# Kernel optimization log

Measured on AMD Instinct MI355X. Metric: run time of the kernel, lower is better.

The kernel has to match this reference:

```python
import jax, jax.numpy as jnp
import numpy as np

NB, FD, NR, L = 4, 128, 4, 4
CUT, CUT3, NE = 5.0, 4.0, 108
N_ATOMS, N_EDGES, N_ANGLES, N_GRAPHS = 8000, 200000, 400000, 100
BONDS_PER, ANGLES_PER = 2000, 4000

def swish(x):
    return x * jax.nn.sigmoid(x)

def cutoff_fn(r, rc):
    x = r / rc
    return 1.0 - 6.0 * x**5 + 15.0 * x**4 - 10.0 * x**3

def rbf(r):
    # smooth Bessel basis, [E, NR+1]
    n = jnp.arange(1, NR + 2, dtype=r.dtype)
    return jnp.sqrt(2.0 / CUT) * jnp.sin(n * jnp.pi * r[:, None] / CUT) / r[:, None]

def shrb(r, cos_t):
    # spherical-harmonic (Legendre, l=0..3) x radial Bessel (n=1..4) -> [A, 16]
    n = jnp.arange(1, NR + 1, dtype=r.dtype)
    rad = jnp.sin(n * jnp.pi * r[:, None] / CUT3) / r[:, None]
    ang = jnp.stack([jnp.ones_like(cos_t), cos_t, 0.5 * (3.0 * cos_t**2 - 1.0), 0.5 * (5.0 * cos_t**3 - 3.0 * cos_t)], axis=1)
    feat = (rad[:, :, None] * ang[:, None, :]).reshape(r.shape[0], NR * L)
    return feat * cutoff_fn(r, CUT3)[:, None]

def setup_inputs() -> dict:
    key = jax.random.key(0)
    ks = jax.random.split(key, 24)
    def nrm(k, shape, fan):
        return jax.random.normal(k, shape, jnp.float32) / np.sqrt(fan).astype(np.float32)
    return {
        'atomic_numbers': jax.random.randint(ks[0], (N_ATOMS,), 0, NE, jnp.int32),
        'edge_index': jax.random.randint(ks[1], (2, N_EDGES), 0, N_ATOMS, jnp.int32),
        'edge_dist': jax.random.uniform(ks[2], (N_EDGES,), jnp.float32, 0.5, CUT),
        'three_body_indices': jax.random.randint(ks[3], (N_ANGLES, 2), 0, BONDS_PER, jnp.int32),
        'norm_ik': jax.random.uniform(ks[4], (N_ANGLES,), jnp.float32, 0.5, CUT3),
        'cos_angles': jax.random.uniform(ks[5], (N_ANGLES,), jnp.float32, -1.0, 1.0),
        'total_num_bonds': jnp.full((N_GRAPHS,), BONDS_PER, jnp.int32),
        'total_num_angles': jnp.full((N_GRAPHS,), ANGLES_PER, jnp.int32),
        'emb': nrm(ks[6], (NE, FD), 1.0),
        'W_enc': nrm(ks[7], (NR + 1, FD), NR + 1), 'b_enc': jnp.zeros((FD,), jnp.float32),
        'W_angle': nrm(ks[8], (NB, NR * L, FD), NR * L),
        'Wg': nrm(ks[9], (NB, FD, FD), FD), 'bg': jnp.zeros((NB, FD), jnp.float32),
        'W_tb': nrm(ks[10], (NB, FD, FD), FD), 'b_tb': jnp.zeros((NB, FD), jnp.float32),
        'We1': nrm(ks[11], (NB, 3 * FD, FD), 3 * FD), 'be1': jnp.zeros((NB, FD), jnp.float32),
        'We0': nrm(ks[12], (NB, NR + 1, FD), NR + 1),
        'Wa1': nrm(ks[13], (NB, 3 * FD, FD), 3 * FD), 'ba1': jnp.zeros((NB, FD), jnp.float32),
        'Wa0': nrm(ks[14], (NB, NR + 1, FD), NR + 1),
        'W1': nrm(ks[15], (FD, FD), FD), 'b1': jnp.zeros((FD,), jnp.float32),
        'W2': nrm(ks[16], (FD, FD), FD), 'b2': jnp.zeros((FD,), jnp.float32),
        'W3': nrm(ks[17], (FD, 1), FD), 'b3': jnp.zeros((1,), jnp.float32),
    }

def reference(atomic_numbers, edge_index, edge_dist, three_body_indices, norm_ik, cos_angles, total_num_bonds, total_num_angles, emb, W_enc, b_enc, W_angle, Wg, bg, W_tb, b_tb, We1, be1, We0, Wa1, ba1, Wa0, W1, b1, W2, b2, W3, b3):
    E, N, A = edge_dist.shape[0], atomic_numbers.shape[0], norm_ik.shape[0]
    # ragged three-body index offsets (cumsum over per-graph bond counts)
    cum = jnp.cumsum(total_num_bonds)
    off = jnp.concatenate([jnp.zeros((1,), cum.dtype), cum[:-1]])
    off_a = jnp.repeat(off, total_num_angles, total_repeat_length=A)
    tbi = three_body_indices + off_a[:, None].astype(three_body_indices.dtype)
    idx_ij, idx_ik = tbi[:, 0], tbi[:, 1]
    send, recv = edge_index[0], edge_index[1]
    ef0 = rbf(edge_dist)                      # [E, 5]
    e = swish(ef0 @ W_enc + b_enc)            # [E, FD]
    v = emb[atomic_numbers]                   # [N, FD]
    ang = shrb(norm_ik, cos_angles)           # [A, 16]
    fc_ik = cutoff_fn(norm_ik, CUT3)          # [A]
    for b in range(NB):
        # three-body interaction: angle -> center bond ij
        k_atom = recv[idx_ik]
        gate = jax.nn.sigmoid(v[k_atom] @ Wg[b] + bg[b])            # [A, FD]
        msg = (ang @ W_angle[b]) * gate * fc_ik[:, None]            # [A, FD]
        agg = jax.ops.segment_sum(msg, idx_ij, num_segments=E)      # [E, FD]
        e = e + swish(agg @ W_tb[b] + b_tb[b])
        # gated graph conv: edge update then atom update
        vi, vj = v[send], v[recv]
        h = jnp.concatenate([vi, vj, e], axis=1)                    # [E, 3FD]
        e = e + swish(h @ We1[b] + be1[b]) * (ef0 @ We0[b])
        h2 = jnp.concatenate([vi, vj, e], axis=1)
        m = swish(h2 @ Wa1[b] + ba1[b]) * (ef0 @ Wa0[b])
        v = v + jax.ops.segment_sum(m, recv, num_segments=N)
    # per-atom energy readout
    h = swish(v @ W1 + b1)
    h = swish(h @ W2 + b2)
    return h @ W3 + b3                                              # [N, 1]
```

## Files before the change

kernel.cpp:

```cpp
#include <hip/hip_runtime.h>


typedef short short8 __attribute__((ext_vector_type(8)));
typedef float f32x4v __attribute__((ext_vector_type(4)));
typedef __bf16 bf16x2_t __attribute__((ext_vector_type(2)));

__device__ __forceinline__ float sigmoidf_(float x) { return 1.0f / (1.0f + __expf(-x)); }
__device__ __forceinline__ float swishf_(float x) { return x * sigmoidf_(x); }

__device__ __forceinline__ unsigned int pk2(float a, float b) {
    bf16x2_t v = {(__bf16)a, (__bf16)b};
    return __builtin_bit_cast(unsigned int, v);
}
__device__ __forceinline__ unsigned short f2bf(float x) {
    return __builtin_bit_cast(unsigned short, (__bf16)x);
}
__device__ __forceinline__ float bf2f(unsigned short u) {
    return __uint_as_float(((unsigned int)u) << 16);
}
__device__ __forceinline__ float blo(unsigned int u) { return __uint_as_float(u << 16); }
__device__ __forceinline__ float bhi(unsigned int u) { return __uint_as_float(u & 0xffff0000u); }
__device__ __forceinline__ unsigned int addbf2(unsigned int a, unsigned int b) {
    return pk2(blo(a) + blo(b), bhi(a) + bhi(b));
}

__device__ __forceinline__ f32x4v mfma_bf16(short8 a, short8 b, f32x4v c) {
    return __builtin_amdgcn_mfma_f32_16x16x32_bf16(a, b, c, 0, 0, 0);
}

__device__ __forceinline__ float4 f4add(float4 a, float4 b) {
    return make_float4(a.x + b.x, a.y + b.y, a.z + b.z, a.w + b.w);
}
__device__ __forceinline__ float4 f4swish(float4 a) {
    return make_float4(swishf_(a.x), swishf_(a.y), swishf_(a.z), swishf_(a.w));
}
__device__ __forceinline__ float getc(const float4& v, int i) {
    return i == 0 ? v.x : (i == 1 ? v.y : (i == 2 ? v.z : v.w));
}

#define FMA4(J, A) \
    acc[J].x = fmaf(A, bv.x, acc[J].x); acc[J].y = fmaf(A, bv.y, acc[J].y); \
    acc[J].z = fmaf(A, bv.z, acc[J].z); acc[J].w = fmaf(A, bv.w, acc[J].w)

template <int S>
__device__ __forceinline__ void gemm32f(const float* As, const float* __restrict__ B,
                                        int tm, int f0, float4 acc[4]) {
#pragma unroll 4
    for (int k = 0; k < 128; ++k) {
        const float4 a0 = *(const float4*)(As + k * S + (tm << 2));
        const float4 bv = *(const float4*)(B + (k << 7) + f0);
        FMA4(0, a0.x); FMA4(1, a0.y); FMA4(2, a0.z); FMA4(3, a0.w);
    }
}

__global__ void k_offsets(const int* __restrict__ tnb, const int* __restrict__ tna,
                          int NG, int* __restrict__ boff, int* __restrict__ acum) {
    if (threadIdx.x == 0 && blockIdx.x == 0) {
        int ab = 0, aa = 0;
        for (int g = 0; g < NG; ++g) {
            boff[g] = ab;
            ab += tnb[g];
            aa += tna[g];
            acum[g] = aa;
        }
    }
}

__global__ void k_angle_setup(const int* __restrict__ tb, const float* __restrict__ rnorm,
                              const float* __restrict__ cosang, const int* __restrict__ ei,
                              int E, int A, int NG,
                              const int* __restrict__ boff, const int* __restrict__ acum,
                              unsigned short* __restrict__ ang,
                              int* __restrict__ kat, int* __restrict__ iij,
                              int* __restrict__ cnt) {
    const int a = blockIdx.x * 256 + threadIdx.x;
    if (a >= A) return;
    int lo = 0, hi = NG - 1;
    while (lo < hi) {
        const int mid = (lo + hi) >> 1;
        if (a < acum[mid]) hi = mid; else lo = mid + 1;
    }
    const int off = boff[lo];
    iij[a] = tb[2 * a] + off;
    kat[a] = ei[(size_t)E + tb[2 * a + 1] + off];
    atomicAdd(&cnt[tb[2 * a] + off], 1);

    const float r = rnorm[a], c = cosang[a];
    const float rinv = 1.0f / r;
    const float x = r * 0.25f;
    const float fc = 1.0f + x * x * x * (-10.0f + x * (15.0f - 6.0f * x));
    const float fc2 = fc * fc;
    const float p2 = 1.5f * c * c - 0.5f;
    const float p3 = 2.5f * c * c * c - 1.5f * c;
    union { unsigned int ui[8]; uint4 v[2]; } pkk;
#pragma unroll
    for (int n = 0; n < 4; ++n) {
        const float rad = __sinf(r * (float)(n + 1) * 0.7853981633974483f) * rinv * fc2;
        pkk.ui[n * 2 + 0] = pk2(rad, rad * c);
        pkk.ui[n * 2 + 1] = pk2(rad * p2, rad * p3);
    }
    uint4* ap = (uint4*)(ang + (size_t)a * 16);
    ap[0] = pkk.v[0];
    ap[1] = pkk.v[1];
}

__global__ void k_scan1(const int* __restrict__ cnt, int* __restrict__ start,
                        int* __restrict__ bsum, int n) {
    __shared__ int sh[256];
    const int t = threadIdx.x;
    const int base = blockIdx.x * 2048 + t * 8;
    int v[8], s = 0;
#pragma unroll
    for (int i = 0; i < 8; ++i) { v[i] = (base + i < n) ? cnt[base + i] : 0; s += v[i]; }
    sh[t] = s;
    __syncthreads();
    for (int off = 1; off < 256; off <<= 1) {
        int x = (t >= off) ? sh[t - off] : 0;
        __syncthreads();
        sh[t] += x;
        __syncthreads();
    }
    if (t == 255) bsum[blockIdx.x] = sh[255];
    int run = sh[t] - s;
#pragma unroll
    for (int i = 0; i < 8; ++i) { if (base + i < n) start[base + i] = run; run += v[i]; }
}

__global__ void k_scan2(int* __restrict__ bsum, int nb) {
    __shared__ int sh[256];
    const int t = threadIdx.x;
    int v = (t < nb) ? bsum[t] : 0;
    sh[t] = v;
    __syncthreads();
    for (int off = 1; off < 256; off <<= 1) {
        int x = (t >= off) ? sh[t - off] : 0;
        __syncthreads();
        sh[t] += x;
        __syncthreads();
    }
    if (t < nb) bsum[t] = sh[t] - v;
}

__global__ void k_scan3(int* __restrict__ start, const int* __restrict__ bsum, int n) {
    const int i = blockIdx.x * 256 + threadIdx.x;
    if (i < n) start[i] += bsum[i >> 11];
}

__global__ void k_scatter(const unsigned short* __restrict__ ang,
                          const int* __restrict__ kat, const int* __restrict__ iij,
                          const int* __restrict__ start, int* __restrict__ fill,
                          unsigned short* __restrict__ angS, int* __restrict__ katS, int A) {
    const int a = blockIdx.x * 256 + threadIdx.x;
    if (a >= A) return;
    const int ij = iij[a];
    const int pos = start[ij] + atomicAdd(&fill[ij], 1);
    const uint4* src = (const uint4*)(ang + (size_t)a * 16);
    uint4* dst = (uint4*)(angS + (size_t)pos * 16);
    dst[0] = src[0];
    dst[1] = src[1];
    katS[pos] = kat[a];
}

__global__ void k_scatter_recv(const int* __restrict__ ei, int E,
                               const int* __restrict__ startR, int* __restrict__ fillR,
                               int* __restrict__ epos) {
    const int e = blockIdx.x * 256 + threadIdx.x;
    if (e < E) {
        const int r = ei[(size_t)E + e];
        epos[e] = startR[r] + atomicAdd(&fillR[r], 1);
    }
}

__global__ void k_pack(const float* __restrict__ Wg, const float* __restrict__ Wtb,
                       const float* __restrict__ We1, const float* __restrict__ Wa1,
                       unsigned short* __restrict__ Bpk) {
    const int gid = blockIdx.x * 256 + threadIdx.x;
    const int mat = gid >> 11;
    const int t2 = gid & 2047;
    const int b = mat >> 3, which = mat & 7;
    const float* W;
    switch (which) {
        case 0: W = Wg + (size_t)b * 16384; break;
        case 1: W = We1 + (size_t)b * 49152; break;
        case 2: W = We1 + (size_t)b * 49152 + 16384; break;
        case 3: W = Wa1 + (size_t)b * 49152; break;
        case 4: W = Wa1 + (size_t)b * 49152 + 16384; break;
        case 5: W = Wtb + (size_t)b * 16384; break;
        case 6: W = We1 + (size_t)b * 49152 + 32768; break;
        default: W = Wa1 + (size_t)b * 49152 + 32768; break;
    }
    const int kc = t2 >> 9, nt = (t2 >> 6) & 7, lane = t2 & 63;
    const int q = lane >> 4, cc = lane & 15;
    const int col = nt * 16 + cc;
    union { unsigned short us[8]; uint4 v; } pk;
#pragma unroll
    for (int j = 0; j < 8; ++j)
        pk.us[j] = f2bf(W[(size_t)(kc * 32 + q * 8 + j) * 128 + col]);
    *(uint4*)(Bpk + (size_t)mat * 16384 + (size_t)((kc * 8 + nt) * 64 + lane) * 8) = pk.v;
}

__global__ void k_pack_s(const float* __restrict__ Wang, const float* __restrict__ We0g,
                         const float* __restrict__ Wa0g, unsigned short* __restrict__ Spk) {
    const int gid = blockIdx.x * 64 + threadIdx.x;
    const int m = gid >> 9;
    const int nt = (gid >> 6) & 7, lane = gid & 63;
    const int b = m & 3, type = m >> 2;
    const int q = lane >> 4, cc = lane & 15;
    const int col = nt * 16 + cc;
    const float* W;
    int K;
    if (type == 0)      { W = Wang + (size_t)b * 2048; K = 16; }
    else if (type == 1) { W = We0g + (size_t)b * 640;  K = 5;  }
    else                { W = Wa0g + (size_t)b * 640;  K = 5;  }
    union { unsigned short us[8]; uint4 v; } pk;
#pragma unroll
    for (int j = 0; j < 8; ++j) {
        const int k = q * 8 + j;
        pk.us[j] = (k < K) ? f2bf(W[(size_t)k * 128 + col]) : (unsigned short)0;
    }
    *(uint4*)(Spk + (size_t)m * 4096 + (size_t)(nt * 64 + lane) * 8) = pk.v;
}

__global__ void k_edge_init(const float* __restrict__ dist, const float* __restrict__ Wenc,
                            const float* __restrict__ benc,
                            const int* __restrict__ ei, int E, int* __restrict__ cntR,
                            unsigned int* __restrict__ ePq,
                            unsigned int* __restrict__ ef0q) {
    __shared__ float sarr[16][5];
    const int s = blockIdx.x, t = threadIdx.x;
    if (t < 16) {
        const float r = dist[s * 16 + t];
        const float rinv = 1.0f / r;
        float vv[5];
#pragma unroll
        for (int n = 0; n < 5; ++n) {
            vv[n] = 0.6324555320336759f * __sinf(r * (float)(n + 1) * 0.6283185307179586f) * rinv;
            sarr[t][n] = vv[n];
        }
        uint4 pq;
        pq.x = pk2(vv[0], vv[1]);
        pq.y = pk2(vv[2], vv[3]);
        pq.z = pk2(vv[4], 0.0f);
        pq.w = 0u;
        *(uint4*)(ef0q + (size_t)(s * 16 + t) * 4) = pq;
        atomicAdd(&cntR[ei[(size_t)E + s * 16 + t]], 1);
    }
    __syncthreads();
    const int lane = t >> 3, nt = t & 7;
    const int q = lane >> 4;
    const int f = nt * 16 + (lane & 15);
    float wv[5];
#pragma unroll
    for (int n = 0; n < 5; ++n) wv[n] = Wenc[n * 128 + f];
    const float bz = benc[f];
    float o[4];
#pragma unroll
    for (int r = 0; r < 4; ++r) {
        const int m = q * 4 + r;
        float acc = bz;
#pragma unroll
        for (int n = 0; n < 5; ++n) acc = fmaf(sarr[m][n], wv[n], acc);
        o[r] = swishf_(acc);
    }
    unsigned int* epB = ePq + (size_t)s * 1024;
    epB[(nt * 2) * 64 + lane] = pk2(o[0], o[1]);
    epB[(nt * 2 + 1) * 64 + lane] = pk2(o[2], o[3]);
}

__global__ void k_atom_init(const int* __restrict__ an, const float* __restrict__ emb,
                            float* __restrict__ v, unsigned int* __restrict__ vq, int N) {
    const size_t gid = (size_t)blockIdx.x * 256 + threadIdx.x;
    if (gid >= (size_t)N * 64) return;
    const int a = (int)(gid >> 6), j = (int)(gid & 63);
    const float2 e = *(const float2*)(emb + (size_t)an[a] * 128 + 2 * j);
    *(float2*)(v + (size_t)a * 128 + 2 * j) = e;
    vq[gid] = pk2(e.x, e.y);
}

__global__ void __launch_bounds__(256, 4) k_atom_pre(
    const unsigned int* __restrict__ vq,
    const unsigned short* __restrict__ Bpk5, const float* __restrict__ bg,
    unsigned int* __restrict__ Gq, unsigned int* __restrict__ Pe1q,
    unsigned int* __restrict__ Pe2q,
    unsigned int* __restrict__ Pa1q, unsigned int* __restrict__ Pa2q) {
    __shared__ __align__(16) unsigned short At[64 * 136];
    unsigned int* At32 = (unsigned int*)At;
    const int t = threadIdx.x;
    const int w = t >> 6, l = t & 63;
    const int q = l >> 4, c = l & 15;
    const int g = blockIdx.y;
    const int abase = blockIdx.x * 64 + 16 * w;

    const unsigned short* vh = (const unsigned short*)vq;
    short8 af[4];
#pragma unroll
    for (int kc = 0; kc < 4; ++kc)
        af[kc] = *(const short8*)(vh + (size_t)(abase + c) * 128 + kc * 32 + q * 8);

    const short8* Bp = (const short8*)(Bpk5 + (size_t)g * 16384);
    const f32x4v zz = {0.0f, 0.0f, 0.0f, 0.0f};
    f32x4v acc[8];
#pragma unroll
    for (int nt = 0; nt < 8; ++nt) acc[nt] = zz;
#pragma unroll
    for (int nt = 0; nt < 8; ++nt)
#pragma unroll
        for (int kc = 0; kc < 4; ++kc)
            acc[nt] = mfma_bf16(af[kc], Bp[(kc * 8 + nt) * 64 + l], acc[nt]);

    unsigned int* OUT = (g == 0) ? Gq : (g == 1) ? Pe1q : (g == 2) ? Pe2q
                      : (g == 3) ? Pa1q : Pa2q;
#pragma unroll
    for (int nt = 0; nt < 8; ++nt) {
        const int fo = nt * 16 + c;
        if (g == 0) {
            const float bz = bg[fo];
#pragma unroll
            for (int r = 0; r < 4; ++r)
                At[(16 * w + q * 4 + r) * 136 + fo] = f2bf(sigmoidf_(acc[nt][r] + bz));
        } else {
#pragma unroll
            for (int r = 0; r < 4; ++r)
                At[(16 * w + q * 4 + r) * 136 + fo] = f2bf(acc[nt][r]);
        }
    }
#pragma unroll
    for (int j = 0; j < 16; ++j)
        OUT[(size_t)(abase + j) * 64 + l] = At32[(16 * w + j) * 68 + l];
}

__global__ void __launch_bounds__(128, 4) k_edge(
    const unsigned short* __restrict__ angBS, const int* __restrict__ katS,
    const int* __restrict__ startA, const int* __restrict__ cntA,
    const unsigned int* __restrict__ Gq, const unsigned short* __restrict__ Wangpk,
    const unsigned int* __restrict__ ef0q,
    unsigned int* __restrict__ ePq, const int* __restrict__ ei, int E,
    const unsigned int* __restrict__ Pe1q, const unsigned int* __restrict__ Pe2q,
    const unsigned int* __restrict__ Pa1q, const unsigned int* __restrict__ Pa2q,
    const int* __restrict__ epos,
    const unsigned short* __restrict__ Bpk3,
    const float* __restrict__ btb, const float* __restrict__ be1,
    const unsigned short* __restrict__ We0pk, const float* __restrict__ ba1,
    const unsigned short* __restrict__ Wa0pk, unsigned int* __restrict__ mPq) {
    __shared__ __align__(16) unsigned short At[32 * 136];
    __shared__ __align__(16) unsigned short sPh[32 * 136];
    __shared__ int sA0[32], sAn[32];
    unsigned int* At32 = (unsigned int*)At;
    unsigned int* sP32 = (unsigned int*)sPh;

    const int t = threadIdx.x;
    const int w = t >> 6, l = t & 63;
    const int q = l >> 4, c = l & 15;
    const int g4 = l >> 4, l16 = l & 15;
    const size_t base = (size_t)blockIdx.x * 32;
    const int wbase = (int)base + 16 * w;
    const f32x4v zz = {0.0f, 0.0f, 0.0f, 0.0f};

    if (l < 16) {
        sA0[16 * w + l] = startA[wbase + l];
        sAn[16 * w + l] = cntA[wbase + l];
    }

    int eiS[4], eiR[4];
#pragma unroll
    for (int i = 0; i < 4; ++i) {
        eiS[i] = ei[wbase + i * 4 + g4];
        eiR[i] = ei[(size_t)E + wbase + i * 4 + g4];
    }

    short8 afE = {0, 0, 0, 0, 0, 0, 0, 0};
    if (q == 0)
        afE = *(const short8*)((const unsigned short*)ef0q + (size_t)(wbase + c) * 8);

#define STAGE_SP(P1, P2)                                                         \
    _Pragma("unroll") for (int i = 0; i < 4; ++i) {                              \
        const int j = i * 4 + g4;                                                \
        const uint4 u1 = *(const uint4*)((P1) + (size_t)eiS[i] * 64 + l16 * 4);  \
        const uint4 u2 = *(const uint4*)((P2) + (size_t)eiR[i] * 64 + l16 * 4);  \
        uint4 o;                                                                 \
        o.x = addbf2(u1.x, u2.x); o.y = addbf2(u1.y, u2.y);                      \
        o.z = addbf2(u1.z, u2.z); o.w = addbf2(u1.w, u2.w);                      \
        *(uint4*)(sP32 + (16 * w + j) * 68 + l16 * 4) = o;                       \
    }

    unsigned int* epB = ePq + (size_t)(blockIdx.x * 2 + w) * 1024;

    {
        int j = 0;
        const int aBeg = __builtin_amdgcn_readfirstlane(sA0[16 * w]);
        const int aEnd = __builtin_amdgcn_readfirstlane(sA0[16 * w + 15] + sAn[16 * w + 15]);
        int nextB = __builtin_amdgcn_readfirstlane(sA0[16 * w] + sAn[16 * w]);
        float aa0 = 0.0f, aa1 = 0.0f;
        const short8* WB = (const short8*)Wangpk;
        unsigned short* msg = sPh + (16 * w) * 136;
        unsigned int* msg32 = sP32 + (16 * w) * 68;

#define FLUSH_TO(AIDX)                                                           \
        while ((AIDX) >= nextB && j < 15) {                                      \
            At32[(16 * w + j) * 68 + l] = pk2(aa0, aa1);                         \
            aa0 = 0.0f; aa1 = 0.0f;                                              \
            ++j;                                                                 \
            nextB = __builtin_amdgcn_readfirstlane(sA0[16 * w + j] + sAn[16 * w + j]); \
        }

        short8 afN = {0, 0, 0, 0, 0, 0, 0, 0};
        if (aBeg < aEnd && q < 2 && aBeg + c < aEnd)
            afN = *(const short8*)(angBS + (size_t)(aBeg + c) * 16 + q * 8);

        for (int a0 = aBeg; a0 < aEnd; a0 += 16) {
            const short8 afA = afN;
            short8 afZ = {0, 0, 0, 0, 0, 0, 0, 0};
            afN = afZ;
            if (q < 2 && a0 + 16 + c < aEnd)
                afN = *(const short8*)(angBS + (size_t)(a0 + 16 + c) * 16 + q * 8);

            unsigned int gvv[16];
#pragma unroll
            for (int r16 = 0; r16 < 16; ++r16) {
                const int aa = (a0 + r16 < aEnd) ? a0 + r16 : aEnd - 1;
                gvv[r16] = Gq[(size_t)katS[aa] * 64 + l];
            }

#pragma unroll
            for (int nt = 0; nt < 8; ++nt) {
                f32x4v d = mfma_bf16(afA, WB[nt * 64 + l], zz);
#pragma unroll
                for (int r = 0; r < 4; ++r)
                    msg[(q * 4 + r) * 136 + nt * 16 + c] = f2bf(d[r]);
            }
            asm volatile("s_waitcnt lgkmcnt(0)" ::: "memory");
            __builtin_amdgcn_sched_barrier(0);

            unsigned int mvv[16];
#pragma unroll
            for (int r16 = 0; r16 < 16; ++r16) mvv[r16] = msg32[r16 * 68 + l];
            asm volatile("s_waitcnt lgkmcnt(0)" ::: "memory");
            __builtin_amdgcn_sched_barrier(0);

#pragma unroll
            for (int r16 = 0; r16 < 16; ++r16) {
                const int a = a0 + r16;
                FLUSH_TO(a)
                aa0 = fmaf(blo(mvv[r16]), blo(gvv[r16]), aa0);
                aa1 = fmaf(bhi(mvv[r16]), bhi(gvv[r16]), aa1);
            }
        }
        At32[(16 * w + j) * 68 + l] = pk2(aa0, aa1);
        for (int jj = j + 1; jj < 16; ++jj) At32[(16 * w + jj) * 68 + l] = 0u;
#undef FLUSH_TO
    }
    asm volatile("s_waitcnt lgkmcnt(0)" ::: "memory");
    __builtin_amdgcn_sched_barrier(0);

    STAGE_SP(Pe1q, Pe2q)

    const short8* Bp1 = (const short8*)Bpk3;
    const short8* Bp2 = Bp1 + 2048;
    const short8* Bp3 = Bp2 + 2048;
    const short8* W0e = (const short8*)We0pk;
    const short8* W0a = (const short8*)Wa0pk;

    short8 af[4];
#define LOAD_AF                                                                  \
    _Pragma("unroll") for (int kc = 0; kc < 4; ++kc)                             \
        af[kc] = *(const short8*)(At + (16 * w + c) * 136 + kc * 32 + q * 8);
#define TRANSPOSE_ER2                                                            \
    _Pragma("unroll") for (int nt = 0; nt < 8; ++nt) {                           \
        At[(16 * w + q * 4 + 0) * 136 + nt * 16 + c] = (unsigned short)er2[2 * nt];        \
        At[(16 * w + q * 4 + 1) * 136 + nt * 16 + c] = (unsigned short)(er2[2 * nt] >> 16);\
        At[(16 * w + q * 4 + 2) * 136 + nt * 16 + c] = (unsigned short)er2[2 * nt + 1];    \
        At[(16 * w + q * 4 + 3) * 136 + nt * 16 + c] = (unsigned short)(er2[2 * nt + 1] >> 16);\
    }

    unsigned int er2[16];

    LOAD_AF
#pragma unroll 1
    for (int h = 0; h < 2; ++h) {
        unsigned int eold[8];
#pragma unroll
        for (int s = 0; s < 8; ++s) eold[s] = epB[(h * 8 + s) * 64 + l];
        f32x4v acc[4];
#pragma unroll
        for (int n2 = 0; n2 < 4; ++n2) acc[n2] = zz;
#pragma unroll
        for (int n2 = 0; n2 < 4; ++n2)
#pragma unroll
            for (int kc = 0; kc < 4; ++kc)
                acc[n2] = mfma_bf16(af[kc], Bp1[(kc * 8 + h * 4 + n2) * 64 + l], acc[n2]);
#pragma unroll
        for (int n2 = 0; n2 < 4; ++n2) {
            const int nt = h * 4 + n2;
            const unsigned int e0 = eold[2 * n2];
            const unsigned int e1 = eold[2 * n2 + 1];
            const float bt = btb[nt * 16 + c];
            er2[2 * nt] = pk2(blo(e0) + swishf_(acc[n2][0] + bt),
                              bhi(e0) + swishf_(acc[n2][1] + bt));
            er2[2 * nt + 1] = pk2(blo(e1) + swishf_(acc[n2][2] + bt),
                                  bhi(e1) + swishf_(acc[n2][3] + bt));
        }
    }
    TRANSPOSE_ER2

    asm volatile("s_waitcnt lgkmcnt(0)" ::: "memory");
    __builtin_amdgcn_sched_barrier(0);

    LOAD_AF
#pragma unroll 1
    for (int h = 0; h < 2; ++h) {
        f32x4v acc[4];
#pragma unroll
        for (int n2 = 0; n2 < 4; ++n2) acc[n2] = zz;
#pragma unroll
        for (int n2 = 0; n2 < 4; ++n2)
#pragma unroll
            for (int kc = 0; kc < 4; ++kc)
                acc[n2] = mfma_bf16(af[kc], Bp2[(kc * 8 + h * 4 + n2) * 64 + l], acc[n2]);
        f32x4v scv[4];
#pragma unroll
        for (int n2 = 0; n2 < 4; ++n2)
            scv[n2] = mfma_bf16(afE, W0e[(h * 4 + n2) * 64 + l], zz);
#pragma unroll
        for (int n2 = 0; n2 < 4; ++n2) {
            const int nt = h * 4 + n2;
            const int fo = nt * 16 + c;
            const float bt = be1[fo];
            float vv[4];
#pragma unroll
            for (int r = 0; r < 4; ++r) {
                const float p12 = bf2f(sPh[(16 * w + q * 4 + r) * 136 + fo]);
                const float x = acc[n2][r] + bt + p12;
                const unsigned int eold = er2[2 * nt + (r >> 1)];
                const float eb = (r & 1) ? bhi(eold) : blo(eold);
                vv[r] = eb + swishf_(x) * scv[n2][r];
            }
            er2[2 * nt] = pk2(vv[0], vv[1]);
            er2[2 * nt + 1] = pk2(vv[2], vv[3]);
            epB[(2 * nt) * 64 + l] = er2[2 * nt];
            epB[(2 * nt + 1) * 64 + l] = er2[2 * nt + 1];
        }
    }
    STAGE_SP(Pa1q, Pa2q)
    TRANSPOSE_ER2

    LOAD_AF
#pragma unroll 1
    for (int h = 0; h < 2; ++h) {
        f32x4v acc[4];
#pragma unroll
        for (int n2 = 0; n2 < 4; ++n2) acc[n2] = zz;
#pragma unroll
        for (int n2 = 0; n2 < 4; ++n2)
#pragma unroll
            for (int kc = 0; kc < 4; ++kc)
                acc[n2] = mfma_bf16(af[kc], Bp3[(kc * 8 + h * 4 + n2) * 64 + l], acc[n2]);
        f32x4v scv[4];
#pragma unroll
        for (int n2 = 0; n2 < 4; ++n2)
            scv[n2] = mfma_bf16(afE, W0a[(h * 4 + n2) * 64 + l], zz);
#pragma unroll
        for (int n2 = 0; n2 < 4; ++n2) {
            const int nt = h * 4 + n2;
            const int fo = nt * 16 + c;
            const float bt = ba1[fo];
#pragma unroll
            for (int r = 0; r < 4; ++r) {
                const float p12 = bf2f(sPh[(16 * w + q * 4 + r) * 136 + fo]);
                const float x = acc[n2][r] + bt + p12;
                At[(16 * w + q * 4 + r) * 136 + fo] = f2bf(swishf_(x) * scv[n2][r]);
            }
        }
    }
#pragma unroll
    for (int j = 0; j < 16; ++j) {
        const int ep = epos[wbase + j];
        mPq[(size_t)ep * 64 + l] = At32[(16 * w + j) * 68 + l];
    }
#undef LOAD_AF
#undef TRANSPOSE_ER2
#undef STAGE_SP
}

__global__ void k_dvagg(const unsigned int* __restrict__ mPq,
                        const int* __restrict__ startR, const int* __restrict__ cntR,
                        float* __restrict__ v, unsigned int* __restrict__ vq, int N) {
    const int a = blockIdx.x * 4 + (threadIdx.x >> 6);
    if (a >= N) return;
    const int l = threadIdx.x & 63;
    const int s0 = startR[a], n = cntR[a];
    float a0 = 0.0f, a1 = 0.0f, b0 = 0.0f, b1 = 0.0f;
    int i = 0;
    for (; i + 4 <= n; i += 4) {
        const unsigned int u0 = mPq[(size_t)(s0 + i + 0) * 64 + l];
        const unsigned int u1 = mPq[(size_t)(s0 + i + 1) * 64 + l];
        const unsigned int u2 = mPq[(size_t)(s0 + i + 2) * 64 + l];
        const unsigned int u3 = mPq[(size_t)(s0 + i + 3) * 64 + l];
        a0 += blo(u0) + blo(u1);
        a1 += bhi(u0) + bhi(u1);
        b0 += blo(u2) + blo(u3);
        b1 += bhi(u2) + bhi(u3);
    }
    for (; i < n; ++i) {
        const unsigned int u = mPq[(size_t)(s0 + i) * 64 + l];
        a0 += blo(u);
        a1 += bhi(u);
    }
    a0 += b0;
    a1 += b1;
    const float v0 = v[(size_t)a * 128 + 2 * l] + a0;
    const float v1 = v[(size_t)a * 128 + 2 * l + 1] + a1;
    v[(size_t)a * 128 + 2 * l] = v0;
    v[(size_t)a * 128 + 2 * l + 1] = v1;
    vq[(size_t)a * 64 + l] = pk2(v0, v1);
}

__global__ void k_readout(const float* __restrict__ v,
                          const float* __restrict__ W1, const float* __restrict__ b1,
                          const float* __restrict__ W2, const float* __restrict__ b2,
                          const float* __restrict__ W3, const float* __restrict__ b3,
                          float* __restrict__ out) {
    __shared__ float At[128 * 36];
    const int t = threadIdx.x;
    const int tn = t & 31, tm = t >> 5;
    const int f0 = tn << 2;
    const size_t base = (size_t)blockIdx.x * 32;
    {
        const int m = t & 31, cb = t >> 5;
        const float4* src = (const float4*)(v + (base + m) * 128);
#pragma unroll
        for (int i = 0; i < 4; ++i) {
            const int c = cb + (i << 3);
            const float4 ld = src[c];
            float* dst = At + (c << 2) * 32 + m;
            dst[0] = ld.x; dst[32] = ld.y; dst[64] = ld.z; dst[96] = ld.w;
        }
    }
    __syncthreads();
    float4 acc[4] = {};
    gemm32f<32>(At, W1, tm, f0, acc);
    {
        const float4 bv1 = *(const float4*)(b1 + f0);
#pragma unroll
        for (int j = 0; j < 4; ++j) acc[j] = f4swish(f4add(acc[j], bv1));
    }
    __syncthreads();
#pragma unroll
    for (int i = 0; i < 4; ++i) {
        float4 w0;
        w0.x = getc(acc[0], i); w0.y = getc(acc[1], i); w0.z = getc(acc[2], i); w0.w = getc(acc[3], i);
        *(float4*)(At + (f0 + i) * 36 + (tm << 2)) = w0;
    }
    __syncthreads();
    float4 acc2[4] = {};
    gemm32f<36>(At, W2, tm, f0, acc2);
    const float4 bv2 = *(const float4*)(b2 + f0);
    const float4 w3v = *(const float4*)(W3 + f0);
#pragma unroll
    for (int j = 0; j < 4; ++j) {
        const float4 h = f4swish(f4add(acc2[j], bv2));
        float p = h.x * w3v.x + h.y * w3v.y + h.z * w3v.z + h.w * w3v.w;
        p += __shfl_xor(p, 16);
        p += __shfl_xor(p, 8);
        p += __shfl_xor(p, 4);
        p += __shfl_xor(p, 2);
        p += __shfl_xor(p, 1);
        if (tn == 0) out[base + (tm << 2) + j] = p + b3[0];
    }
}

extern "C" void kernel_launch(void* const* d_in, const int* in_sizes, int n_in,
                              void* d_out, int out_size, void* d_ws, size_t ws_size,
                              hipStream_t stream) {
    const int N = in_sizes[0];
    const int E = in_sizes[2];
    const int A = in_sizes[4];
    const int NG = in_sizes[6];

    const int* an = (const int*)d_in[0];
    const int* ei = (const int*)d_in[1];
    const float* dist = (const float*)d_in[2];
    const int* tb = (const int*)d_in[3];
    const float* rnorm = (const float*)d_in[4];
    const float* cosang = (const float*)d_in[5];
    const int* tnb = (const int*)d_in[6];
    const int* tna = (const int*)d_in[7];
    const float* emb = (const float*)d_in[8];
    const float* Wenc = (const float*)d_in[9];
    const float* benc = (const float*)d_in[10];
    const float* Wang = (const float*)d_in[11];
    const float* Wg = (const float*)d_in[12];
    const float* bg = (const float*)d_in[13];
    const float* Wtb = (const float*)d_in[14];
    const float* btb = (const float*)d_in[15];
    const float* We1 = (const float*)d_in[16];
    const float* be1 = (const float*)d_in[17];
    const float* We0 = (const float*)d_in[18];
    const float* Wa1 = (const float*)d_in[19];
    const float* ba1 = (const float*)d_in[20];
    const float* Wa0 = (const float*)d_in[21];
    const float* W1 = (const float*)d_in[22];
    const float* b1 = (const float*)d_in[23];
    const float* W2 = (const float*)d_in[24];
    const float* b2 = (const float*)d_in[25];
    const float* W3 = (const float*)d_in[26];
    const float* b3 = (const float*)d_in[27];
    float* out = (float*)d_out;

    float* ws = (float*)d_ws;
    size_t off = 0;
    auto alloc = [&](size_t n) { float* p = ws + off; off += (n + 3) & ~(size_t)3; return p; };
    unsigned int* ePq = (unsigned int*)alloc((size_t)E * 64);
    unsigned int* mPq = (unsigned int*)alloc((size_t)E * 64);
    float* v_ = alloc((size_t)N * 128);
    unsigned int* vq = (unsigned int*)alloc((size_t)N * 64);
    unsigned int* Gq = (unsigned int*)alloc((size_t)N * 64);
    unsigned int* Pe1q = (unsigned int*)alloc((size_t)N * 64);
    unsigned int* Pe2q = (unsigned int*)alloc((size_t)N * 64);
    unsigned int* Pa1q = (unsigned int*)alloc((size_t)N * 64);
    unsigned int* Pa2q = (unsigned int*)alloc((size_t)N * 64);
    unsigned int* ef0q = (unsigned int*)alloc((size_t)E * 4);
    unsigned short* angB = (unsigned short*)alloc((size_t)A * 8);
    unsigned short* angBS = (unsigned short*)alloc((size_t)A * 8);
    int* kat = (int*)alloc((size_t)A);
    int* katS = (int*)alloc((size_t)A);
    int* iij = (int*)alloc((size_t)A);
    int* cnt = (int*)alloc((size_t)E);
    int* start = (int*)alloc((size_t)E);
    int* fill = (int*)alloc((size_t)E);
    int* cntR = (int*)alloc((size_t)N);
    int* startR = (int*)alloc((size_t)N);
    int* fillR = (int*)alloc((size_t)N);
    int* epos = (int*)alloc((size_t)E);
    int* bsum = (int*)alloc(512);
    int* boff = (int*)alloc(256);
    int* acum = boff + 128;
    unsigned short* Bpk = (unsigned short*)alloc((size_t)32 * 8192);
    unsigned short* Spk = (unsigned short*)alloc((size_t)12 * 2048);

    const int nscanE = (E + 2047) / 2048;
    const int nscanR = (N + 2047) / 2048;

    (void)hipMemsetAsync(cnt, 0, (size_t)E * 4, stream);
    (void)hipMemsetAsync(fill, 0, (size_t)E * 4, stream);
    (void)hipMemsetAsync(cntR, 0, (size_t)N * 4, stream);
    (void)hipMemsetAsync(fillR, 0, (size_t)N * 4, stream);
    k_offsets<<<1, 64, 0, stream>>>(tnb, tna, NG, boff, acum);
    k_angle_setup<<<(A + 255) / 256, 256, 0, stream>>>(tb, rnorm, cosang, ei, E, A, NG,
                                                       boff, acum, angB, kat, iij, cnt);
    k_edge_init<<<E / 16, 512, 0, stream>>>(dist, Wenc, benc, ei, E, cntR, ePq, ef0q);
    k_scan1<<<nscanE, 256, 0, stream>>>(cnt, start, bsum, E);
    k_scan2<<<1, 256, 0, stream>>>(bsum, nscanE);
    k_scan3<<<(E + 255) / 256, 256, 0, stream>>>(start, bsum, E);
    k_scatter<<<(A + 255) / 256, 256, 0, stream>>>(angB, kat, iij, start, fill, angBS, katS, A);
    k_scan1<<<nscanR, 256, 0, stream>>>(cntR, startR, bsum, N);
    k_scan2<<<1, 256, 0, stream>>>(bsum, nscanR);
    k_scan3<<<(N + 255) / 256, 256, 0, stream>>>(startR, bsum, N);
    k_scatter_recv<<<(E + 255) / 256, 256, 0, stream>>>(ei, E, startR, fillR, epos);
    k_pack<<<256, 256, 0, stream>>>(Wg, Wtb, We1, Wa1, Bpk);
    k_pack_s<<<96, 64, 0, stream>>>(Wang, We0, Wa0, Spk);
    k_atom_init<<<(int)(((size_t)N * 64 + 255) / 256), 256, 0, stream>>>(an, emb, v_, vq, N);

    for (int b = 0; b < 4; ++b) {
        k_atom_pre<<<dim3(N / 64, 5), 256, 0, stream>>>(
            vq, Bpk + (size_t)(b * 8) * 16384, bg + b * 128,
            Gq, Pe1q, Pe2q, Pa1q, Pa2q);
        k_edge<<<E / 32, 128, 0, stream>>>(
            angBS, katS, start, cnt, Gq, Spk + (size_t)b * 4096, ef0q,
            ePq, ei, E, Pe1q, Pe2q, Pa1q, Pa2q, epos,
            Bpk + (size_t)(b * 8 + 5) * 16384,
            btb + b * 128, be1 + b * 128,
            Spk + (size_t)(4 + b) * 4096, ba1 + b * 128,
            Spk + (size_t)(8 + b) * 4096, mPq);
        k_dvagg<<<(N + 3) / 4, 256, 0, stream>>>(mPq, startR, cntR, v_, vq, N);
    }
    k_readout<<<N / 32, 256, 0, stream>>>(v_, W1, b1, W2, b2, W3, b3, out);
}
```

Measured before the change: 959.1 us.

## Software-pipeline angle message MFMA with gate gathers and accumulation in k_edge

Restructures the three-body aggregation loop in k_edge into a two-stage software pipeline. Message tiles now alternate between two LDS buffers, and the gate gathers for the next chunk are issued while the previous chunk is being accumulated. The goal is to hide global gather latency and LDS round-trips behind the MFMA work. In exchange it adds a third 32x136 shared buffer, which raises LDS use per block and may reduce occupancy, and it holds more live registers.

```diff
diff --git a/kernel.cpp b/kernel.cpp
--- a/kernel.cpp
+++ b/kernel.cpp
@@ -344,6 +344,7 @@
     const unsigned short* __restrict__ Wa0pk, unsigned int* __restrict__ mPq) {
     __shared__ __align__(16) unsigned short At[32 * 136];
     __shared__ __align__(16) unsigned short sPh[32 * 136];
+    __shared__ __align__(16) unsigned short sMsg[32 * 136];
     __shared__ int sA0[32], sAn[32];
     unsigned int* At32 = (unsigned int*)At;
     unsigned int* sP32 = (unsigned int*)sPh;
@@ -392,8 +393,10 @@
         int nextB = __builtin_amdgcn_readfirstlane(sA0[16 * w] + sAn[16 * w]);
         float aa0 = 0.0f, aa1 = 0.0f;
         const short8* WB = (const short8*)Wangpk;
-        unsigned short* msg = sPh + (16 * w) * 136;
-        unsigned int* msg32 = sP32 + (16 * w) * 68;
+        unsigned short* msg0 = sPh + (16 * w) * 136;
+        unsigned short* msg1 = sMsg + (16 * w) * 136;
+        unsigned int* m32_0 = sP32 + (16 * w) * 68;
+        unsigned int* m32_1 = (unsigned int*)sMsg + (16 * w) * 68;
 
 #define FLUSH_TO(AIDX)                                                           \
         while ((AIDX) >= nextB && j < 15) {                                      \
@@ -406,7 +409,17 @@
         short8 afN = {0, 0, 0, 0, 0, 0, 0, 0};
         if (aBeg < aEnd && q < 2 && aBeg + c < aEnd)
             afN = *(const short8*)(angBS + (size_t)(aBeg + c) * 16 + q * 8);
-
+        unsigned int gvvP[16], mvvP[16];
+        if (aBeg < aEnd) {
+#pragma unroll
+            for (int r16 = 0; r16 < 16; ++r16) {
+                const int aa = (aBeg + r16 < aEnd) ? aBeg + r16 : aEnd - 1;
+                gvvP[r16] = Gq[(size_t)katS[aa] * 64 + l];
+            }
+        }
+
+        int aPrev = -1;
+        int phase = 0;
         for (int a0 = aBeg; a0 < aEnd; a0 += 16) {
             const short8 afA = afN;
             short8 afZ = {0, 0, 0, 0, 0, 0, 0, 0};
@@ -414,35 +427,47 @@
             if (q < 2 && a0 + 16 + c < aEnd)
                 afN = *(const short8*)(angBS + (size_t)(a0 + 16 + c) * 16 + q * 8);
 
-            unsigned int gvv[16];
-#pragma unroll
-            for (int r16 = 0; r16 < 16; ++r16) {
-                const int aa = (a0 + r16 < aEnd) ? a0 + r16 : aEnd - 1;
-                gvv[r16] = Gq[(size_t)katS[aa] * 64 + l];
-            }
-
+            unsigned short* m = phase ? msg1 : msg0;
 #pragma unroll
             for (int nt = 0; nt < 8; ++nt) {
                 f32x4v d = mfma_bf16(afA, WB[nt * 64 + l], zz);
 #pragma unroll
                 for (int r = 0; r < 4; ++r)
-                    msg[(q * 4 + r) * 136 + nt * 16 + c] = f2bf(d[r]);
+                    m[(q * 4 + r) * 136 + nt * 16 + c] = f2bf(d[r]);
             }
+
+            if (aPrev >= 0) {
+#pragma unroll
+                for (int r16 = 0; r16 < 16; ++r16) {
+                    const int a = aPrev + r16;
+                    FLUSH_TO(a)
+                    aa0 = fmaf(blo(mvvP[r16]), blo(gvvP[r16]), aa0);
+                    aa1 = fmaf(bhi(mvvP[r16]), bhi(gvvP[r16]), aa1);
+                }
+#pragma unroll
+                for (int r16 = 0; r16 < 16; ++r16) {
+                    const int aa = (a0 + r16 < aEnd) ? a0 + r16 : aEnd - 1;
+                    gvvP[r16] = Gq[(size_t)katS[aa] * 64 + l];
+                }
+            }
+
             asm volatile("s_waitcnt lgkmcnt(0)" ::: "memory");
             __builtin_amdgcn_sched_barrier(0);
 
-            unsigned int mvv[16];
-#pragma unroll
-            for (int r16 = 0; r16 < 16; ++r16) mvv[r16] = msg32[r16 * 68 + l];
-            asm volatile("s_waitcnt lgkmcnt(0)" ::: "memory");
-            __builtin_amdgcn_sched_barrier(0);
-
+            unsigned int* m32 = phase ? m32_1 : m32_0;
+#pragma unroll
+            for (int r16 = 0; r16 < 16; ++r16) mvvP[r16] = m32[r16 * 68 + l];
+
+            aPrev = a0;
+            phase ^= 1;
+        }
+        if (aPrev >= 0) {
 #pragma unroll
             for (int r16 = 0; r16 < 16; ++r16) {
-                const int a = a0 + r16;
+                const int a = aPrev + r16;
                 FLUSH_TO(a)
-                aa0 = fmaf(blo(mvv[r16]), blo(gvv[r16]), aa0);
-                aa1 = fmaf(bhi(mvv[r16]), bhi(gvv[r16]), aa1);
+                aa0 = fmaf(blo(mvvP[r16]), blo(gvvP[r16]), aa0);
+                aa1 = fmaf(bhi(mvvP[r16]), bhi(gvvP[r16]), aa1);
             }
         }
         At32[(16 * w + j) * 68 + l] = pk2(aa0, aa1);
```

Result: slower. 1.378 ms (+43.6%).

## Fuse angle setup into scatter and fold block-sum offsets into consumers

Applied to the files above, without the earlier changes.

Splits angle setup into a light histogram pass and a combined pass that computes the angular features and writes them straight to their sorted position. This drops the intermediate unsorted angle, kat and iij buffers and the separate copy kernel. The scan3 kernels are removed, and every consumer (the scatters, k_edge and k_dvagg) adds the per-block scan offset itself. The trade-off is that the binary search over graphs now runs twice and each start lookup needs an extra small indexed load, in exchange for fewer launches and less global memory traffic in setup.

```diff
diff --git a/kernel.cpp b/kernel.cpp
--- a/kernel.cpp
+++ b/kernel.cpp
@@ -66,13 +66,9 @@
     }
 }
 
-__global__ void k_angle_setup(const int* __restrict__ tb, const float* __restrict__ rnorm,
-                              const float* __restrict__ cosang, const int* __restrict__ ei,
-                              int E, int A, int NG,
-                              const int* __restrict__ boff, const int* __restrict__ acum,
-                              unsigned short* __restrict__ ang,
-                              int* __restrict__ kat, int* __restrict__ iij,
-                              int* __restrict__ cnt) {
+__global__ void k_hist_ang(const int* __restrict__ tb,
+                           const int* __restrict__ boff, const int* __restrict__ acum,
+                           int A, int NG, int* __restrict__ cnt) {
     const int a = blockIdx.x * 256 + threadIdx.x;
     if (a >= A) return;
     int lo = 0, hi = NG - 1;
@@ -80,10 +76,28 @@
         const int mid = (lo + hi) >> 1;
         if (a < acum[mid]) hi = mid; else lo = mid + 1;
     }
+    atomicAdd(&cnt[tb[2 * a] + boff[lo]], 1);
+}
+
+__global__ void k_angle_scatter(const int* __restrict__ tb, const float* __restrict__ rnorm,
+                                const float* __restrict__ cosang, const int* __restrict__ ei,
+                                int E, int A, int NG,
+                                const int* __restrict__ boff, const int* __restrict__ acum,
+                                const int* __restrict__ start, const int* __restrict__ bsumE,
+                                int* __restrict__ fill,
+                                unsigned short* __restrict__ angS,
+                                int* __restrict__ katS) {
+    const int a = blockIdx.x * 256 + threadIdx.x;
+    if (a >= A) return;
+    int lo = 0, hi = NG - 1;
+    while (lo < hi) {
+        const int mid = (lo + hi) >> 1;
+        if (a < acum[mid]) hi = mid; else lo = mid + 1;
+    }
     const int off = boff[lo];
-    iij[a] = tb[2 * a] + off;
-    kat[a] = ei[(size_t)E + tb[2 * a + 1] + off];
-    atomicAdd(&cnt[tb[2 * a] + off], 1);
+    const int ij = tb[2 * a] + off;
+    const int kat = ei[(size_t)E + tb[2 * a + 1] + off];
+    const int pos = start[ij] + bsumE[ij >> 11] + atomicAdd(&fill[ij], 1);
 
     const float r = rnorm[a], c = cosang[a];
     const float rinv = 1.0f / r;
@@ -99,9 +113,10 @@
         pkk.ui[n * 2 + 0] = pk2(rad, rad * c);
         pkk.ui[n * 2 + 1] = pk2(rad * p2, rad * p3);
     }
-    uint4* ap = (uint4*)(ang + (size_t)a * 16);
-    ap[0] = pkk.v[0];
-    ap[1] = pkk.v[1];
+    uint4* dst = (uint4*)(angS + (size_t)pos * 16);
+    dst[0] = pkk.v[0];
+    dst[1] = pkk.v[1];
+    katS[pos] = kat;
 }
 
 __global__ void k_scan1(const int* __restrict__ cnt, int* __restrict__ start,
@@ -141,33 +156,14 @@
     if (t < nb) bsum[t] = sh[t] - v;
 }
 
-__global__ void k_scan3(int* __restrict__ start, const int* __restrict__ bsum, int n) {
-    const int i = blockIdx.x * 256 + threadIdx.x;
-    if (i < n) start[i] += bsum[i >> 11];
-}
-
-__global__ void k_scatter(const unsigned short* __restrict__ ang,
-                          const int* __restrict__ kat, const int* __restrict__ iij,
-                          const int* __restrict__ start, int* __restrict__ fill,
-                          unsigned short* __restrict__ angS, int* __restrict__ katS, int A) {
-    const int a = blockIdx.x * 256 + threadIdx.x;
-    if (a >= A) return;
-    const int ij = iij[a];
-    const int pos = start[ij] + atomicAdd(&fill[ij], 1);
-    const uint4* src = (const uint4*)(ang + (size_t)a * 16);
-    uint4* dst = (uint4*)(angS + (size_t)pos * 16);
-    dst[0] = src[0];
-    dst[1] = src[1];
-    katS[pos] = kat[a];
-}
-
 __global__ void k_scatter_recv(const int* __restrict__ ei, int E,
-                               const int* __restrict__ startR, int* __restrict__ fillR,
+                               const int* __restrict__ startR, const int* __restrict__ bsumR,
+                               int* __restrict__ fillR,
                                int* __restrict__ epos) {
     const int e = blockIdx.x * 256 + threadIdx.x;
     if (e < E) {
         const int r = ei[(size_t)E + e];
-        epos[e] = startR[r] + atomicAdd(&fillR[r], 1);
+        epos[e] = startR[r] + bsumR[r >> 11] + atomicAdd(&fillR[r], 1);
     }
 }
 
@@ -331,7 +327,8 @@
 
 __global__ void __launch_bounds__(128, 4) k_edge(
     const unsigned short* __restrict__ angBS, const int* __restrict__ katS,
-    const int* __restrict__ startA, const int* __restrict__ cntA,
+    const int* __restrict__ startA, const int* __restrict__ bsumE,
+    const int* __restrict__ cntA,
     const unsigned int* __restrict__ Gq, const unsigned short* __restrict__ Wangpk,
     const unsigned int* __restrict__ ef0q,
     unsigned int* __restrict__ ePq, const int* __restrict__ ei, int E,
@@ -357,8 +354,9 @@
     const f32x4v zz = {0.0f, 0.0f, 0.0f, 0.0f};
 
     if (l < 16) {
-        sA0[16 * w + l] = startA[wbase + l];
-        sAn[16 * w + l] = cntA[wbase + l];
+        const int e = wbase + l;
+        sA0[16 * w + l] = startA[e] + bsumE[e >> 11];
+        sAn[16 * w + l] = cntA[e];
     }
 
     int eiS[4], eiR[4];
@@ -582,12 +580,13 @@
 }
 
 __global__ void k_dvagg(const unsigned int* __restrict__ mPq,
-                        const int* __restrict__ startR, const int* __restrict__ cntR,
+                        const int* __restrict__ startR, const int* __restrict__ bsumR,
+                        const int* __restrict__ cntR,
                         float* __restrict__ v, unsigned int* __restrict__ vq, int N) {
     const int a = blockIdx.x * 4 + (threadIdx.x >> 6);
     if (a >= N) return;
     const int l = threadIdx.x & 63;
-    const int s0 = startR[a], n = cntR[a];
+    const int s0 = startR[a] + bsumR[a >> 11], n = cntR[a];
     float a0 = 0.0f, a1 = 0.0f, b0 = 0.0f, b1 = 0.0f;
     int i = 0;
     for (; i + 4 <= n; i += 4) {
@@ -719,11 +718,8 @@
     unsigned int* Pa1q = (unsigned int*)alloc((size_t)N * 64);
     unsigned int* Pa2q = (unsigned int*)alloc((size_t)N * 64);
     unsigned int* ef0q = (unsigned int*)alloc((size_t)E * 4);
-    unsigned short* angB = (unsigned short*)alloc((size_t)A * 8);
     unsigned short* angBS = (unsigned short*)alloc((size_t)A * 8);
-    int* kat = (int*)alloc((size_t)A);
     int* katS = (int*)alloc((size_t)A);
-    int* iij = (int*)alloc((size_t)A);
     int* cnt = (int*)alloc((size_t)E);
     int* start = (int*)alloc((size_t)E);
     int* fill = (int*)alloc((size_t)E);
@@ -731,7 +727,8 @@
     int* startR = (int*)alloc((size_t)N);
     int* fillR = (int*)alloc((size_t)N);
     int* epos = (int*)alloc((size_t)E);
-    int* bsum = (int*)alloc(512);
+    int* bsumE = (int*)alloc(512);
+    int* bsumR = (int*)alloc(512);
     int* boff = (int*)alloc(256);
     int* acum = boff + 128;
     unsigned short* Bpk = (unsigned short*)alloc((size_t)32 * 8192);
@@ -745,17 +742,16 @@
     (void)hipMemsetAsync(cntR, 0, (size_t)N * 4, stream);
     (void)hipMemsetAsync(fillR, 0, (size_t)N * 4, stream);
     k_offsets<<<1, 64, 0, stream>>>(tnb, tna, NG, boff, acum);
-    k_angle_setup<<<(A + 255) / 256, 256, 0, stream>>>(tb, rnorm, cosang, ei, E, A, NG,
-                                                       boff, acum, angB, kat, iij, cnt);
+    k_hist_ang<<<(A + 255) / 256, 256, 0, stream>>>(tb, boff, acum, A, NG, cnt);
     k_edge_init<<<E / 16, 512, 0, stream>>>(dist, Wenc, benc, ei, E, cntR, ePq, ef0q);
-    k_scan1<<<nscanE, 256, 0, stream>>>(cnt, start, bsum, E);
-    k_scan2<<<1, 256, 0, stream>>>(bsum, nscanE);
-    k_scan3<<<(E + 255) / 256, 256, 0, stream>>>(start, bsum, E);
-    k_scatter<<<(A + 255) / 256, 256, 0, stream>>>(angB, kat, iij, start, fill, angBS, katS, A);
-    k_scan1<<<nscanR, 256, 0, stream>>>(cntR, startR, bsum, N);
-    k_scan2<<<1, 256, 0, stream>>>(bsum, nscanR);
-    k_scan3<<<(N + 255) / 256, 256, 0, stream>>>(startR, bsum, N);
-    k_scatter_recv<<<(E + 255) / 256, 256, 0, stream>>>(ei, E, startR, fillR, epos);
+    k_scan1<<<nscanE, 256, 0, stream>>>(cnt, start, bsumE, E);
+    k_scan2<<<1, 256, 0, stream>>>(bsumE, nscanE);
+    k_angle_scatter<<<(A + 255) / 256, 256, 0, stream>>>(tb, rnorm, cosang, ei, E, A, NG,
+                                                         boff, acum, start, bsumE, fill,
+                                                         angBS, katS);
+    k_scan1<<<nscanR, 256, 0, stream>>>(cntR, startR, bsumR, N);
+    k_scan2<<<1, 256, 0, stream>>>(bsumR, nscanR);
+    k_scatter_recv<<<(E + 255) / 256, 256, 0, stream>>>(ei, E, startR, bsumR, fillR, epos);
     k_pack<<<256, 256, 0, stream>>>(Wg, Wtb, We1, Wa1, Bpk);
     k_pack_s<<<96, 64, 0, stream>>>(Wang, We0, Wa0, Spk);
     k_atom_init<<<(int)(((size_t)N * 64 + 255) / 256), 256, 0, stream>>>(an, emb, v_, vq, N);
@@ -765,13 +761,13 @@
             vq, Bpk + (size_t)(b * 8) * 16384, bg + b * 128,
             Gq, Pe1q, Pe2q, Pa1q, Pa2q);
         k_edge<<<E / 32, 128, 0, stream>>>(
-            angBS, katS, start, cnt, Gq, Spk + (size_t)b * 4096, ef0q,
+            angBS, katS, start, bsumE, cnt, Gq, Spk + (size_t)b * 4096, ef0q,
             ePq, ei, E, Pe1q, Pe2q, Pa1q, Pa2q, epos,
             Bpk + (size_t)(b * 8 + 5) * 16384,
             btb + b * 128, be1 + b * 128,
             Spk + (size_t)(4 + b) * 4096, ba1 + b * 128,
             Spk + (size_t)(8 + b) * 4096, mPq);
-        k_dvagg<<<(N + 3) / 4, 256, 0, stream>>>(mPq, startR, cntR, v_, vq, N);
+        k_dvagg<<<(N + 3) / 4, 256, 0, stream>>>(mPq, startR, bsumR, cntR, v_, vq, N);
     }
     k_readout<<<N / 32, 256, 0, stream>>>(v_, W1, b1, W2, b2, W3, b3, out);
 }
```

Result: no change. 958.3 us, median of 2 (-0.1%).
